# Performance work log

Measured on AMD Instinct MI355X. Metric: run time of the kernel, lower is better.

The kernel has to match this reference:

```python
import jax, jax.numpy as jnp
import numpy as np

D_EMB = 1024
D_HEAD = 64
B = 4
T = 4096


def setup_inputs() -> dict:
    key = jax.random.key(0)
    kx, kk, kq, kv = jax.random.split(key, 4)
    s = 1.0 / np.sqrt(D_EMB)  # torch Linear default init scale (uniform bound)
    x = jax.random.normal(kx, (B, T, D_EMB), dtype=jnp.float32)
    Wk = jax.random.uniform(kk, (D_HEAD, D_EMB), jnp.float32, -s, s)
    Wq = jax.random.uniform(kq, (D_HEAD, D_EMB), jnp.float32, -s, s)
    Wv = jax.random.uniform(kv, (D_HEAD, D_EMB), jnp.float32, -s, s)
    return {"x": x, "Wk": Wk, "Wq": Wq, "Wv": Wv}


def reference(x, Wk, Wq, Wv):
    # x: (B, T, d_emb); W*: (d_head, d_emb) -- torch Linear stores (out, in)
    k = jnp.einsum('bte,he->bth', x, Wk)
    q = jnp.einsum('bte,he->bth', x, Wq)
    v = jnp.einsum('bte,he->bth', x, Wv)
    scale = D_HEAD ** (-0.5)
    a = jnp.einsum('bth,bsh->bts', q, k) * scale  # (B, T, T)
    Tlen = x.shape[-2]
    causal = jnp.tril(jnp.ones((Tlen, Tlen), dtype=bool))
    a = jnp.where(causal, a, -jnp.inf)
    a = jax.nn.softmax(a, axis=-1)
    return jnp.einsum('bts,bsh->bth', a, v)  # (B, T, d_head)
```

## Files before the change

### kernel.cpp

```cpp
#include <hip/hip_runtime.h>
#include <hip/hip_bf16.h>

#define D_EMB 1024
#define T_LEN 4096
#define NTASK 1088

typedef short short8 __attribute__((ext_vector_type(8)));
typedef float f32x4 __attribute__((ext_vector_type(4)));
typedef float f32x16 __attribute__((ext_vector_type(16)));
typedef float float4v __attribute__((ext_vector_type(4)));

__device__ __forceinline__ unsigned short f32_to_bf16(float f) {
    union { float f; unsigned int u; } c; c.f = f;
    unsigned int u = c.u;
    return (unsigned short)((u + 0x7FFFu + ((u >> 16) & 1u)) >> 16);
}
__device__ __forceinline__ float bf16_to_f32(unsigned short v) {
    union { unsigned int u; float f; } c; c.u = ((unsigned int)v) << 16;
    return c.f;
}
__device__ __forceinline__ unsigned cvtpk_bf16(float a, float b) {
    unsigned r;
    asm("v_cvt_pk_bf16_f32 %0, %1, %2" : "=v"(r) : "v"(a), "v"(b));
    return r;
}
__device__ __forceinline__ void gl_lds16(const void* g, void* l) {
    __builtin_amdgcn_global_load_lds(
        (const __attribute__((address_space(1))) unsigned int*)(g),
        (__attribute__((address_space(3))) unsigned int*)(l), 16, 0, 0);
}

#define QSCALE (0.125f * 1.44269504f)

__global__ __launch_bounds__(256) void convert_w(const float* __restrict__ Wk,
                                                 const float* __restrict__ Wq,
                                                 const float* __restrict__ Wv,
                                                 unsigned short* __restrict__ Wb) {
    int e = (blockIdx.x * 256 + threadIdx.x) * 8;
    const float* src;
    if (e < 65536) src = Wk + e;
    else if (e < 131072) src = Wq + (e - 65536);
    else src = Wv + (e - 131072);
    float4v a0 = *(const float4v*)src;
    float4v a1 = *(const float4v*)(src + 4);
    short8 r;
    r[0] = (short)f32_to_bf16(a0[0]); r[1] = (short)f32_to_bf16(a0[1]);
    r[2] = (short)f32_to_bf16(a0[2]); r[3] = (short)f32_to_bf16(a0[3]);
    r[4] = (short)f32_to_bf16(a1[0]); r[5] = (short)f32_to_bf16(a1[1]);
    r[6] = (short)f32_to_bf16(a1[2]); r[7] = (short)f32_to_bf16(a1[3]);
    int row = e >> 10;
    int dst = e ^ ((row & 7) << 3);
    *(short8*)(Wb + dst) = r;
}

__global__ __launch_bounds__(256, 2) void qkv_proj(const float* __restrict__ x,
                                                   const unsigned short* __restrict__ Wb,
                                                   unsigned short* __restrict__ Kb,
                                                   unsigned short* __restrict__ Qb,
                                                   unsigned short* __restrict__ Vt) {
    __shared__ __attribute__((aligned(16))) unsigned short Wsl[2][12288];

    int tid = threadIdx.x;
    int lane = tid & 63, wave = tid >> 6;
    int lo = lane & 15, hi = lane >> 4;
    int rg = wave >> 1, nh = wave & 1;
    int row0 = blockIdx.x * 32;

    const float* xp = x + (size_t)(row0 + rg * 16 + lo) * D_EMB + hi * 8;

    f32x4 acc[6];
#pragma unroll
    for (int i = 0; i < 6; i++) acc[i] = (f32x4){0.f, 0.f, 0.f, 0.f};

    float4v xa0 = *(const float4v*)(xp);
    float4v xa1 = *(const float4v*)(xp + 4);
    float4v xa2 = *(const float4v*)(xp + 32);
    float4v xa3 = *(const float4v*)(xp + 36);
    float4v xb0 = *(const float4v*)(xp + 64);
    float4v xb1 = *(const float4v*)(xp + 68);
    float4v xb2 = *(const float4v*)(xp + 96);
    float4v xb3 = *(const float4v*)(xp + 100);

#pragma unroll
    for (int j = 0; j < 6; j++) {
        int unit = j * 4 + wave;
        int u = unit * 64 + lane;
        gl_lds16(Wb + (size_t)(u >> 3) * D_EMB + (u & 7) * 8, &Wsl[0][unit * 512]);
    }
    __syncthreads();

    int buf = 0;
    int xorm = (lo & 7) << 4;
    int rowbase = nh * 96 + lo;

    for (int kt = 0; kt < 16; kt++) {
        int ktn = (kt < 14) ? kt + 2 : 15;
        const float* pn = xp + ktn * 64;
        float4v xc0 = *(const float4v*)(pn);
        float4v xc1 = *(const float4v*)(pn + 4);
        float4v xc2 = *(const float4v*)(pn + 32);
        float4v xc3 = *(const float4v*)(pn + 36);

        if (kt < 15) {
            int k0n = (kt + 1) * 64;
#pragma unroll
            for (int j = 0; j < 6; j++) {
                int unit = j * 4 + wave;
                int u = unit * 64 + lane;
                gl_lds16(Wb + (size_t)(u >> 3) * D_EMB + k0n + (u & 7) * 8,
                         &Wsl[buf ^ 1][unit * 512]);
            }
        }

        short8 af[2];
        {
            union { unsigned u[4]; short8 s; } c;
            c.u[0] = cvtpk_bf16(xa0[0], xa0[1]);
            c.u[1] = cvtpk_bf16(xa0[2], xa0[3]);
            c.u[2] = cvtpk_bf16(xa1[0], xa1[1]);
            c.u[3] = cvtpk_bf16(xa1[2], xa1[3]);
            af[0] = c.s;
            c.u[0] = cvtpk_bf16(xa2[0], xa2[1]);
            c.u[1] = cvtpk_bf16(xa2[2], xa2[3]);
            c.u[2] = cvtpk_bf16(xa3[0], xa3[1]);
            c.u[3] = cvtpk_bf16(xa3[2], xa3[3]);
            af[1] = c.s;
        }

        const char* sb = (const char*)&Wsl[buf][0];
#pragma unroll
        for (int i = 0; i < 6; i++) {
            int row = rowbase + i * 16;
#pragma unroll
            for (int ks = 0; ks < 2; ks++) {
                short8 bfrag = *(const short8*)(sb + row * 128 + ((ks * 64 + hi * 16) ^ xorm));
                acc[i] = __builtin_amdgcn_mfma_f32_16x16x32_bf16(af[ks], bfrag, acc[i], 0, 0, 0);
            }
        }
        __syncthreads();
        buf ^= 1;
        xa0 = xb0; xa1 = xb1; xa2 = xb2; xa3 = xb3;
        xb0 = xc0; xb1 = xc1; xb2 = xc2; xb3 = xc3;
    }

#pragma unroll
    for (int i = 0; i < 6; i++) {
        int n = nh * 6 + i;
#pragma unroll
        for (int r = 0; r < 4; r++) {
            int grow = row0 + rg * 16 + hi * 4 + r;
            float val = acc[i][r];
            if (n < 4) {
                Kb[(size_t)grow * 64 + n * 16 + lo] = f32_to_bf16(val);
            } else if (n < 8) {
                Qb[(size_t)grow * 64 + (n - 4) * 16 + lo] = f32_to_bf16(val * QSCALE);
            } else {
                int bb = grow >> 12;
                Vt[((size_t)bb * 64 + (n - 8) * 16 + lo) * T_LEN + (grow & 4095)] = f32_to_bf16(val);
            }
        }
    }
}

__global__ __launch_bounds__(64, 4) void attn(const unsigned short* __restrict__ Qb,
                                              const unsigned short* __restrict__ Kb,
                                              const unsigned short* __restrict__ Vt,
                                              unsigned short* __restrict__ Opart,
                                              float* __restrict__ Mpart,
                                              float* __restrict__ Lpart) {
    int lane = threadIdx.x;
    int q32 = lane & 31;
    int hi = lane >> 5;
    unsigned lin = blockIdx.x;
    int b = lin & 3;
    int s = (int)(((lin >> 3) << 1) | ((lin >> 2) & 1));

    int k = 15, rem = s;
    while (rem >= 8 * (k + 1)) { rem -= 8 * (k + 1); k--; }
    int cpt = k + 1;
    int ti = rem / cpt;
    int t = (k << 3) + 7 - ti;
    int c = rem - ti * cpt;

    int u0 = c * 8;
    int u1 = min(u0 + 8, t + 1);

    size_t base = (size_t)b * T_LEN;
    int qg = t * 32 + q32;

    short8 qf[4];
    const unsigned short* qp = Qb + (base + qg) * 64 + hi * 8;
#pragma unroll
    for (int d = 0; d < 4; d++) qf[d] = *(const short8*)(qp + d * 16);

    size_t vbase = ((size_t)b * 64 + q32) * T_LEN;
    f32x16 o0 = {0.f}, o1 = {0.f};
    float m = -3e38f, l = 0.f;

    for (int u = u0; u < u1; ++u) {
        const unsigned short* kp = Kb + (base + u * 32 + q32) * 64 + hi * 8;
        short8 kc0 = *(const short8*)kp;
        short8 kc1 = *(const short8*)(kp + 16);
        short8 kc2 = *(const short8*)(kp + 32);
        short8 kc3 = *(const short8*)(kp + 48);
        const unsigned short* vp = Vt + vbase + u * 32 + hi * 8;
        short8 vc0 = *(const short8*)vp;
        short8 vc1 = *(const short8*)(vp + 16);
        short8 vc2 = *(const short8*)(vp + 32 * T_LEN);
        short8 vc3 = *(const short8*)(vp + 32 * T_LEN + 16);

        f32x16 sc = {0.f};
        sc = __builtin_amdgcn_mfma_f32_32x32x16_bf16(kc0, qf[0], sc, 0, 0, 0);
        sc = __builtin_amdgcn_mfma_f32_32x32x16_bf16(kc1, qf[1], sc, 0, 0, 0);
        sc = __builtin_amdgcn_mfma_f32_32x32x16_bf16(kc2, qf[2], sc, 0, 0, 0);
        sc = __builtin_amdgcn_mfma_f32_32x32x16_bf16(kc3, qf[3], sc, 0, 0, 0);

        if (u == t) {
#pragma unroll
            for (int r = 0; r < 16; ++r) {
                int ko = (r & 3) + 8 * (r >> 2) + 4 * hi;
                sc[r] = (ko <= q32) ? sc[r] : -3e38f;
            }
        }

        float t0 = fmaxf(fmaxf(sc[0], sc[1]), sc[2]);
        float t1 = fmaxf(fmaxf(sc[3], sc[4]), sc[5]);
        float t2 = fmaxf(fmaxf(sc[6], sc[7]), sc[8]);
        float t3 = fmaxf(fmaxf(sc[9], sc[10]), sc[11]);
        float t4 = fmaxf(fmaxf(sc[12], sc[13]), sc[14]);
        float t5 = fmaxf(fmaxf(t0, t1), sc[15]);
        float t6 = fmaxf(fmaxf(t2, t3), t4);
        float mx = fmaxf(t5, t6);
        mx = fmaxf(mx, __shfl_xor(mx, 32));

        if (__any(mx > m + 8.0f)) {
            float mn = fmaxf(m, mx);
            float al = exp2f(m - mn);
            m = mn; l *= al;
#pragma unroll
            for (int r = 0; r < 16; ++r) { o0[r] *= al; o1[r] *= al; }
        }

#pragma unroll
        for (int r = 0; r < 16; ++r) sc[r] = exp2f(sc[r] - m);
        float y0 = (sc[0] + sc[8]) + (sc[4] + sc[12]);
        float y1 = (sc[1] + sc[9]) + (sc[5] + sc[13]);
        float y2 = (sc[2] + sc[10]) + (sc[6] + sc[14]);
        float y3 = (sc[3] + sc[11]) + (sc[7] + sc[15]);
        float sum = (y0 + y1) + (y2 + y3);
        sum += __shfl_xor(sum, 32);
        l += sum;

        unsigned bb0, bb1, bb2, bb3, bb4, bb5, bb6, bb7;
        bb0 = cvtpk_bf16(sc[0],  sc[1]);
        bb1 = cvtpk_bf16(sc[2],  sc[3]);
        bb2 = cvtpk_bf16(sc[4],  sc[5]);
        bb3 = cvtpk_bf16(sc[6],  sc[7]);
        bb4 = cvtpk_bf16(sc[8],  sc[9]);
        bb5 = cvtpk_bf16(sc[10], sc[11]);
        bb6 = cvtpk_bf16(sc[12], sc[13]);
        bb7 = cvtpk_bf16(sc[14], sc[15]);
        asm("v_permlane32_swap_b32 %0, %1" : "+v"(bb0), "+v"(bb2));
        asm("v_permlane32_swap_b32 %0, %1" : "+v"(bb1), "+v"(bb3));
        asm("v_permlane32_swap_b32 %0, %1" : "+v"(bb4), "+v"(bb6));
        asm("v_permlane32_swap_b32 %0, %1" : "+v"(bb5), "+v"(bb7));
        union U8 { unsigned u[4]; short8 s; };
        U8 p0; p0.u[0] = bb0; p0.u[1] = bb1; p0.u[2] = bb2; p0.u[3] = bb3;
        U8 p1; p1.u[0] = bb4; p1.u[1] = bb5; p1.u[2] = bb6; p1.u[3] = bb7;

        o0 = __builtin_amdgcn_mfma_f32_32x32x16_bf16(vc0, p0.s, o0, 0, 0, 0);
        o0 = __builtin_amdgcn_mfma_f32_32x32x16_bf16(vc1, p1.s, o0, 0, 0, 0);
        o1 = __builtin_amdgcn_mfma_f32_32x32x16_bf16(vc2, p0.s, o1, 0, 0, 0);
        o1 = __builtin_amdgcn_mfma_f32_32x32x16_bf16(vc3, p1.s, o1, 0, 0, 0);
    }

    size_t tbase = ((size_t)(b * NTASK + s) * 32 + q32) * 64;
#pragma unroll
    for (int hb = 0; hb < 2; hb++) {
#pragma unroll
        for (int g = 0; g < 4; g++) {
            float e0 = hb ? o1[4 * g] : o0[4 * g];
            float e1 = hb ? o1[4 * g + 1] : o0[4 * g + 1];
            float e2 = hb ? o1[4 * g + 2] : o0[4 * g + 2];
            float e3 = hb ? o1[4 * g + 3] : o0[4 * g + 3];
            unsigned w0 = cvtpk_bf16(e0, e1);
            unsigned w1 = cvtpk_bf16(e2, e3);
            int h0 = hb * 32 + g * 8 + hi * 4;
            *reinterpret_cast<uint2*>(Opart + tbase + h0) = make_uint2(w0, w1);
        }
    }
    if (lane < 32) {
        Mpart[(b * NTASK + s) * 32 + q32] = m;
        Lpart[(b * NTASK + s) * 32 + q32] = l;
    }
}

__global__ __launch_bounds__(256) void attn_merge(const unsigned short* __restrict__ Opart,
                                                  const float* __restrict__ Mpart,
                                                  const float* __restrict__ Lpart,
                                                  float* __restrict__ out) {
    int tid = threadIdx.x;
    int g = blockIdx.x * 64 + (tid >> 2);
    int h0 = (tid & 3) * 16;
    int b = g >> 12, t = g & 4095;
    int tile = t >> 5, r32 = t & 31;
    int k = tile >> 3;
    int nch = k + 1;
    int s0 = 8 * (136 - (((k + 1) * (k + 2)) >> 1)) + (7 - (tile & 7)) * nch;
    int tb = b * NTASK + s0;

    float mm = -3e38f;
    for (int i = 0; i < nch; i++) mm = fmaxf(mm, Mpart[(tb + i) * 32 + r32]);
    float ll = 0.f;
    float acc[16];
#pragma unroll
    for (int e = 0; e < 16; e++) acc[e] = 0.f;
    for (int i = 0; i < nch; i++) {
        float a = exp2f(Mpart[(tb + i) * 32 + r32] - mm);
        ll += a * Lpart[(tb + i) * 32 + r32];
        const unsigned short* op = Opart + ((size_t)(tb + i) * 32 + r32) * 64 + h0;
        short8 v0 = *(const short8*)op;
        short8 v1 = *(const short8*)(op + 8);
#pragma unroll
        for (int e = 0; e < 8; e++) {
            acc[e]     += a * bf16_to_f32((unsigned short)v0[e]);
            acc[8 + e] += a * bf16_to_f32((unsigned short)v1[e]);
        }
    }
    float inv = 1.f / ll;
    float* dst = out + (size_t)g * 64 + h0;
#pragma unroll
    for (int e = 0; e < 16; e++) dst[e] = acc[e] * inv;
}

extern "C" void kernel_launch(void* const* d_in, const int* in_sizes, int n_in,
                              void* d_out, int out_size, void* d_ws, size_t ws_size,
                              hipStream_t stream) {
    (void)in_sizes; (void)n_in; (void)out_size; (void)ws_size;
    const float* x  = (const float*)d_in[0];
    const float* Wk = (const float*)d_in[1];
    const float* Wq = (const float*)d_in[2];
    const float* Wv = (const float*)d_in[3];
    float* out = (float*)d_out;

    unsigned short* Wb = (unsigned short*)d_ws;
    unsigned short* Kb = Wb + 196608;
    unsigned short* Qb = Kb + 1048576;
    unsigned short* Vt = Qb + 1048576;
    unsigned short* Opart = Vt + 1048576;
    float* Mpart = (float*)(Opart + (size_t)4 * NTASK * 32 * 64);
    float* Lpart = Mpart + 4 * NTASK * 32;

    hipLaunchKernelGGL(convert_w, dim3(96), dim3(256), 0, stream, Wk, Wq, Wv, Wb);
    hipLaunchKernelGGL(qkv_proj, dim3(512), dim3(256), 0, stream, x, Wb, Kb, Qb, Vt);
    hipLaunchKernelGGL(attn, dim3(4 * NTASK), dim3(64), 0, stream, Qb, Kb, Vt, Opart, Mpart, Lpart);
    hipLaunchKernelGGL(attn_merge, dim3(256), dim3(256), 0, stream, Opart, Mpart, Lpart, out);
}
```

Baseline: 93.14 us.

## Process two 32-row query tiles per attention wave to reuse K/V loads

Each attention wave now handles a 64-row query supertile, two 32-row tiles, instead of one. Every K and V chunk loaded from global memory feeds MFMAs for both tiles, halving K/V traffic per query and giving the scheduler independent MFMA chains to interleave. The task decomposition, causal masking, partial-result slot layout and merge indexing are rewritten to match. The cost is roughly double the register pressure, reflected in launch bounds dropping from 4 to 2 waves. Half as many blocks are launched, each doing some wasted masked work on the diagonal chunk for tile A.

```diff
diff --git a/kernel.cpp b/kernel.cpp
--- a/kernel.cpp
+++ b/kernel.cpp
@@ -3,7 +3,7 @@
 
 #define D_EMB 1024
 #define T_LEN 4096
-#define NTASK 1088
+#define NTASK2 544
 
 typedef short short8 __attribute__((ext_vector_type(8)));
 typedef float f32x4 __attribute__((ext_vector_type(4)));
@@ -23,6 +23,12 @@
     unsigned r;
     asm("v_cvt_pk_bf16_f32 %0, %1, %2" : "=v"(r) : "v"(a), "v"(b));
     return r;
+}
+__device__ __forceinline__ float xhalf_max(float x) {
+    return fmaxf(x, __shfl_xor(x, 32));
+}
+__device__ __forceinline__ float xhalf_add(float x) {
+    return x + __shfl_xor(x, 32);
 }
 __device__ __forceinline__ void gl_lds16(const void* g, void* l) {
     __builtin_amdgcn_global_load_lds(
@@ -162,7 +168,7 @@
     }
 }
 
-__global__ __launch_bounds__(64, 4) void attn(const unsigned short* __restrict__ Qb,
+__global__ __launch_bounds__(64, 2) void attn(const unsigned short* __restrict__ Qb,
                                               const unsigned short* __restrict__ Kb,
                                               const unsigned short* __restrict__ Vt,
                                               unsigned short* __restrict__ Opart,
@@ -175,27 +181,32 @@
     int b = lin & 3;
     int s = (int)(((lin >> 3) << 1) | ((lin >> 2) & 1));
 
-    int k = 15, rem = s;
-    while (rem >= 8 * (k + 1)) { rem -= 8 * (k + 1); k--; }
-    int cpt = k + 1;
-    int ti = rem / cpt;
-    int t = (k << 3) + 7 - ti;
-    int c = rem - ti * cpt;
+    int k = 16, rem = s;
+    while (rem >= 4 * k) { rem -= 4 * k; k--; }
+    int ti = rem / k;
+    int st = 4 * k - 1 - ti;
+    int c = rem - ti * k;
 
     int u0 = c * 8;
-    int u1 = min(u0 + 8, t + 1);
+    int u1 = min(u0 + 8, 2 * st + 2);
+    int ta = 2 * st, tb = ta + 1;
+    int qrowA = 64 * st + q32;
+    int qrowB = qrowA + 32;
 
     size_t base = (size_t)b * T_LEN;
-    int qg = t * 32 + q32;
-
-    short8 qf[4];
-    const unsigned short* qp = Qb + (base + qg) * 64 + hi * 8;
-#pragma unroll
-    for (int d = 0; d < 4; d++) qf[d] = *(const short8*)(qp + d * 16);
+
+    short8 qfa[4], qfb[4];
+    const unsigned short* qpa = Qb + (base + qrowA) * 64 + hi * 8;
+    const unsigned short* qpb = Qb + (base + qrowB) * 64 + hi * 8;
+#pragma unroll
+    for (int d = 0; d < 4; d++) {
+        qfa[d] = *(const short8*)(qpa + d * 16);
+        qfb[d] = *(const short8*)(qpb + d * 16);
+    }
 
     size_t vbase = ((size_t)b * 64 + q32) * T_LEN;
-    f32x16 o0 = {0.f}, o1 = {0.f};
-    float m = -3e38f, l = 0.f;
+    f32x16 oA0 = {0.f}, oA1 = {0.f}, oB0 = {0.f}, oB1 = {0.f};
+    float mA = -3e38f, lA = 0.f, mB = -3e38f, lB = 0.f;
 
     for (int u = u0; u < u1; ++u) {
         const unsigned short* kp = Kb + (base + u * 32 + q32) * 64 + hi * 8;
@@ -209,89 +220,134 @@
         short8 vc2 = *(const short8*)(vp + 32 * T_LEN);
         short8 vc3 = *(const short8*)(vp + 32 * T_LEN + 16);
 
-        f32x16 sc = {0.f};
-        sc = __builtin_amdgcn_mfma_f32_32x32x16_bf16(kc0, qf[0], sc, 0, 0, 0);
-        sc = __builtin_amdgcn_mfma_f32_32x32x16_bf16(kc1, qf[1], sc, 0, 0, 0);
-        sc = __builtin_amdgcn_mfma_f32_32x32x16_bf16(kc2, qf[2], sc, 0, 0, 0);
-        sc = __builtin_amdgcn_mfma_f32_32x32x16_bf16(kc3, qf[3], sc, 0, 0, 0);
-
-        if (u == t) {
+        f32x16 sa = {0.f}, sb = {0.f};
+        sa = __builtin_amdgcn_mfma_f32_32x32x16_bf16(kc0, qfa[0], sa, 0, 0, 0);
+        sb = __builtin_amdgcn_mfma_f32_32x32x16_bf16(kc0, qfb[0], sb, 0, 0, 0);
+        sa = __builtin_amdgcn_mfma_f32_32x32x16_bf16(kc1, qfa[1], sa, 0, 0, 0);
+        sb = __builtin_amdgcn_mfma_f32_32x32x16_bf16(kc1, qfb[1], sb, 0, 0, 0);
+        sa = __builtin_amdgcn_mfma_f32_32x32x16_bf16(kc2, qfa[2], sa, 0, 0, 0);
+        sb = __builtin_amdgcn_mfma_f32_32x32x16_bf16(kc2, qfb[2], sb, 0, 0, 0);
+        sa = __builtin_amdgcn_mfma_f32_32x32x16_bf16(kc3, qfa[3], sa, 0, 0, 0);
+        sb = __builtin_amdgcn_mfma_f32_32x32x16_bf16(kc3, qfb[3], sb, 0, 0, 0);
+
+        if (u >= ta) {
 #pragma unroll
             for (int r = 0; r < 16; ++r) {
-                int ko = (r & 3) + 8 * (r >> 2) + 4 * hi;
-                sc[r] = (ko <= q32) ? sc[r] : -3e38f;
+                int key = 32 * u + (r & 3) + 8 * (r >> 2) + 4 * hi;
+                sa[r] = (key <= qrowA) ? sa[r] : -3e38f;
+                if (u == tb) sb[r] = (key <= qrowB) ? sb[r] : -3e38f;
             }
         }
 
-        float t0 = fmaxf(fmaxf(sc[0], sc[1]), sc[2]);
-        float t1 = fmaxf(fmaxf(sc[3], sc[4]), sc[5]);
-        float t2 = fmaxf(fmaxf(sc[6], sc[7]), sc[8]);
-        float t3 = fmaxf(fmaxf(sc[9], sc[10]), sc[11]);
-        float t4 = fmaxf(fmaxf(sc[12], sc[13]), sc[14]);
-        float t5 = fmaxf(fmaxf(t0, t1), sc[15]);
-        float t6 = fmaxf(fmaxf(t2, t3), t4);
-        float mx = fmaxf(t5, t6);
-        mx = fmaxf(mx, __shfl_xor(mx, 32));
-
-        if (__any(mx > m + 8.0f)) {
-            float mn = fmaxf(m, mx);
-            float al = exp2f(m - mn);
-            m = mn; l *= al;
-#pragma unroll
-            for (int r = 0; r < 16; ++r) { o0[r] *= al; o1[r] *= al; }
-        }
-
-#pragma unroll
-        for (int r = 0; r < 16; ++r) sc[r] = exp2f(sc[r] - m);
-        float y0 = (sc[0] + sc[8]) + (sc[4] + sc[12]);
-        float y1 = (sc[1] + sc[9]) + (sc[5] + sc[13]);
-        float y2 = (sc[2] + sc[10]) + (sc[6] + sc[14]);
-        float y3 = (sc[3] + sc[11]) + (sc[7] + sc[15]);
-        float sum = (y0 + y1) + (y2 + y3);
-        sum += __shfl_xor(sum, 32);
-        l += sum;
-
-        unsigned bb0, bb1, bb2, bb3, bb4, bb5, bb6, bb7;
-        bb0 = cvtpk_bf16(sc[0],  sc[1]);
-        bb1 = cvtpk_bf16(sc[2],  sc[3]);
-        bb2 = cvtpk_bf16(sc[4],  sc[5]);
-        bb3 = cvtpk_bf16(sc[6],  sc[7]);
-        bb4 = cvtpk_bf16(sc[8],  sc[9]);
-        bb5 = cvtpk_bf16(sc[10], sc[11]);
-        bb6 = cvtpk_bf16(sc[12], sc[13]);
-        bb7 = cvtpk_bf16(sc[14], sc[15]);
-        asm("v_permlane32_swap_b32 %0, %1" : "+v"(bb0), "+v"(bb2));
-        asm("v_permlane32_swap_b32 %0, %1" : "+v"(bb1), "+v"(bb3));
-        asm("v_permlane32_swap_b32 %0, %1" : "+v"(bb4), "+v"(bb6));
-        asm("v_permlane32_swap_b32 %0, %1" : "+v"(bb5), "+v"(bb7));
+        float a0 = fmaxf(fmaxf(sa[0], sa[1]), sa[2]);
+        float a1 = fmaxf(fmaxf(sa[3], sa[4]), sa[5]);
+        float a2 = fmaxf(fmaxf(sa[6], sa[7]), sa[8]);
+        float a3 = fmaxf(fmaxf(sa[9], sa[10]), sa[11]);
+        float a4 = fmaxf(fmaxf(sa[12], sa[13]), sa[14]);
+        float mxA = fmaxf(fmaxf(fmaxf(a0, a1), fmaxf(a2, a3)), fmaxf(a4, sa[15]));
+        float b0 = fmaxf(fmaxf(sb[0], sb[1]), sb[2]);
+        float b1 = fmaxf(fmaxf(sb[3], sb[4]), sb[5]);
+        float b2 = fmaxf(fmaxf(sb[6], sb[7]), sb[8]);
+        float b3 = fmaxf(fmaxf(sb[9], sb[10]), sb[11]);
+        float b4 = fmaxf(fmaxf(sb[12], sb[13]), sb[14]);
+        float mxB = fmaxf(fmaxf(fmaxf(b0, b1), fmaxf(b2, b3)), fmaxf(b4, sb[15]));
+        mxA = xhalf_max(mxA);
+        mxB = xhalf_max(mxB);
+
+        float grow = fmaxf(mxA - mA, mxB - mB);
+        if (__any(grow > 8.0f)) {
+            float mnA = fmaxf(mA, mxA);
+            float alA = exp2f(mA - mnA);
+            mA = mnA; lA *= alA;
+            float mnB = fmaxf(mB, mxB);
+            float alB = exp2f(mB - mnB);
+            mB = mnB; lB *= alB;
+#pragma unroll
+            for (int r = 0; r < 16; ++r) {
+                oA0[r] *= alA; oA1[r] *= alA;
+                oB0[r] *= alB; oB1[r] *= alB;
+            }
+        }
+
+#pragma unroll
+        for (int r = 0; r < 16; ++r) {
+            sa[r] = exp2f(sa[r] - mA);
+            sb[r] = exp2f(sb[r] - mB);
+        }
+        float yA = ((sa[0] + sa[8]) + (sa[4] + sa[12])) + ((sa[1] + sa[9]) + (sa[5] + sa[13]))
+                 + ((sa[2] + sa[10]) + (sa[6] + sa[14])) + ((sa[3] + sa[11]) + (sa[7] + sa[15]));
+        float yB = ((sb[0] + sb[8]) + (sb[4] + sb[12])) + ((sb[1] + sb[9]) + (sb[5] + sb[13]))
+                 + ((sb[2] + sb[10]) + (sb[6] + sb[14])) + ((sb[3] + sb[11]) + (sb[7] + sb[15]));
+        lA += xhalf_add(yA);
+        lB += xhalf_add(yB);
+
+        unsigned pa0 = cvtpk_bf16(sa[0],  sa[1]);
+        unsigned pa1 = cvtpk_bf16(sa[2],  sa[3]);
+        unsigned pa2 = cvtpk_bf16(sa[4],  sa[5]);
+        unsigned pa3 = cvtpk_bf16(sa[6],  sa[7]);
+        unsigned pa4 = cvtpk_bf16(sa[8],  sa[9]);
+        unsigned pa5 = cvtpk_bf16(sa[10], sa[11]);
+        unsigned pa6 = cvtpk_bf16(sa[12], sa[13]);
+        unsigned pa7 = cvtpk_bf16(sa[14], sa[15]);
+        unsigned pb0 = cvtpk_bf16(sb[0],  sb[1]);
+        unsigned pb1 = cvtpk_bf16(sb[2],  sb[3]);
+        unsigned pb2 = cvtpk_bf16(sb[4],  sb[5]);
+        unsigned pb3 = cvtpk_bf16(sb[6],  sb[7]);
+        unsigned pb4 = cvtpk_bf16(sb[8],  sb[9]);
+        unsigned pb5 = cvtpk_bf16(sb[10], sb[11]);
+        unsigned pb6 = cvtpk_bf16(sb[12], sb[13]);
+        unsigned pb7 = cvtpk_bf16(sb[14], sb[15]);
+        asm("v_permlane32_swap_b32 %0, %1" : "+v"(pa0), "+v"(pa2));
+        asm("v_permlane32_swap_b32 %0, %1" : "+v"(pa1), "+v"(pa3));
+        asm("v_permlane32_swap_b32 %0, %1" : "+v"(pa4), "+v"(pa6));
+        asm("v_permlane32_swap_b32 %0, %1" : "+v"(pa5), "+v"(pa7));
+        asm("v_permlane32_swap_b32 %0, %1" : "+v"(pb0), "+v"(pb2));
+        asm("v_permlane32_swap_b32 %0, %1" : "+v"(pb1), "+v"(pb3));
+        asm("v_permlane32_swap_b32 %0, %1" : "+v"(pb4), "+v"(pb6));
+        asm("v_permlane32_swap_b32 %0, %1" : "+v"(pb5), "+v"(pb7));
         union U8 { unsigned u[4]; short8 s; };
-        U8 p0; p0.u[0] = bb0; p0.u[1] = bb1; p0.u[2] = bb2; p0.u[3] = bb3;
-        U8 p1; p1.u[0] = bb4; p1.u[1] = bb5; p1.u[2] = bb6; p1.u[3] = bb7;
-
-        o0 = __builtin_amdgcn_mfma_f32_32x32x16_bf16(vc0, p0.s, o0, 0, 0, 0);
-        o0 = __builtin_amdgcn_mfma_f32_32x32x16_bf16(vc1, p1.s, o0, 0, 0, 0);
-        o1 = __builtin_amdgcn_mfma_f32_32x32x16_bf16(vc2, p0.s, o1, 0, 0, 0);
-        o1 = __builtin_amdgcn_mfma_f32_32x32x16_bf16(vc3, p1.s, o1, 0, 0, 0);
-    }
-
-    size_t tbase = ((size_t)(b * NTASK + s) * 32 + q32) * 64;
+        U8 fA0; fA0.u[0] = pa0; fA0.u[1] = pa1; fA0.u[2] = pa2; fA0.u[3] = pa3;
+        U8 fA1; fA1.u[0] = pa4; fA1.u[1] = pa5; fA1.u[2] = pa6; fA1.u[3] = pa7;
+        U8 fB0; fB0.u[0] = pb0; fB0.u[1] = pb1; fB0.u[2] = pb2; fB0.u[3] = pb3;
+        U8 fB1; fB1.u[0] = pb4; fB1.u[1] = pb5; fB1.u[2] = pb6; fB1.u[3] = pb7;
+
+        oA0 = __builtin_amdgcn_mfma_f32_32x32x16_bf16(vc0, fA0.s, oA0, 0, 0, 0);
+        oB0 = __builtin_amdgcn_mfma_f32_32x32x16_bf16(vc0, fB0.s, oB0, 0, 0, 0);
+        oA0 = __builtin_amdgcn_mfma_f32_32x32x16_bf16(vc1, fA1.s, oA0, 0, 0, 0);
+        oB0 = __builtin_amdgcn_mfma_f32_32x32x16_bf16(vc1, fB1.s, oB0, 0, 0, 0);
+        oA1 = __builtin_amdgcn_mfma_f32_32x32x16_bf16(vc2, fA0.s, oA1, 0, 0, 0);
+        oB1 = __builtin_amdgcn_mfma_f32_32x32x16_bf16(vc2, fB0.s, oB1, 0, 0, 0);
+        oA1 = __builtin_amdgcn_mfma_f32_32x32x16_bf16(vc3, fA1.s, oA1, 0, 0, 0);
+        oB1 = __builtin_amdgcn_mfma_f32_32x32x16_bf16(vc3, fB1.s, oB1, 0, 0, 0);
+    }
+
+    int slotA = (b * NTASK2 + s) * 2;
+    size_t tbA = ((size_t)slotA * 32 + q32) * 64;
+    size_t tbB = ((size_t)(slotA + 1) * 32 + q32) * 64;
 #pragma unroll
     for (int hb = 0; hb < 2; hb++) {
 #pragma unroll
         for (int g = 0; g < 4; g++) {
-            float e0 = hb ? o1[4 * g] : o0[4 * g];
-            float e1 = hb ? o1[4 * g + 1] : o0[4 * g + 1];
-            float e2 = hb ? o1[4 * g + 2] : o0[4 * g + 2];
-            float e3 = hb ? o1[4 * g + 3] : o0[4 * g + 3];
-            unsigned w0 = cvtpk_bf16(e0, e1);
-            unsigned w1 = cvtpk_bf16(e2, e3);
+            float eA0 = hb ? oA1[4 * g] : oA0[4 * g];
+            float eA1 = hb ? oA1[4 * g + 1] : oA0[4 * g + 1];
+            float eA2 = hb ? oA1[4 * g + 2] : oA0[4 * g + 2];
+            float eA3 = hb ? oA1[4 * g + 3] : oA0[4 * g + 3];
+            float eB0 = hb ? oB1[4 * g] : oB0[4 * g];
+            float eB1 = hb ? oB1[4 * g + 1] : oB0[4 * g + 1];
+            float eB2 = hb ? oB1[4 * g + 2] : oB0[4 * g + 2];
+            float eB3 = hb ? oB1[4 * g + 3] : oB0[4 * g + 3];
             int h0 = hb * 32 + g * 8 + hi * 4;
-            *reinterpret_cast<uint2*>(Opart + tbase + h0) = make_uint2(w0, w1);
+            *reinterpret_cast<uint2*>(Opart + tbA + h0) =
+                make_uint2(cvtpk_bf16(eA0, eA1), cvtpk_bf16(eA2, eA3));
+            *reinterpret_cast<uint2*>(Opart + tbB + h0) =
+                make_uint2(cvtpk_bf16(eB0, eB1), cvtpk_bf16(eB2, eB3));
         }
     }
     if (lane < 32) {
-        Mpart[(b * NTASK + s) * 32 + q32] = m;
-        Lpart[(b * NTASK + s) * 32 + q32] = l;
+        Mpart[slotA * 32 + q32] = mA;
+        Lpart[slotA * 32 + q32] = lA;
+        Mpart[(slotA + 1) * 32 + q32] = mB;
+        Lpart[(slotA + 1) * 32 + q32] = lB;
     }
 }
 
@@ -303,22 +359,25 @@
     int g = blockIdx.x * 64 + (tid >> 2);
     int h0 = (tid & 3) * 16;
     int b = g >> 12, t = g & 4095;
-    int tile = t >> 5, r32 = t & 31;
-    int k = tile >> 3;
-    int nch = k + 1;
-    int s0 = 8 * (136 - (((k + 1) * (k + 2)) >> 1)) + (7 - (tile & 7)) * nch;
-    int tb = b * NTASK + s0;
+    int tile32 = t >> 5, r32 = t & 31;
+    int st = tile32 >> 1, member = tile32 & 1;
+    int k = (st >> 2) + 1;
+    int sbase = 4 * (136 - ((k * (k + 1)) >> 1));
+    int ti = 4 * k - 1 - st;
+    int s0 = sbase + ti * k;
+    int slot0 = (b * NTASK2 + s0) * 2 + member;
 
     float mm = -3e38f;
-    for (int i = 0; i < nch; i++) mm = fmaxf(mm, Mpart[(tb + i) * 32 + r32]);
+    for (int i = 0; i < k; i++) mm = fmaxf(mm, Mpart[(slot0 + 2 * i) * 32 + r32]);
     float ll = 0.f;
     float acc[16];
 #pragma unroll
     for (int e = 0; e < 16; e++) acc[e] = 0.f;
-    for (int i = 0; i < nch; i++) {
-        float a = exp2f(Mpart[(tb + i) * 32 + r32] - mm);
-        ll += a * Lpart[(tb + i) * 32 + r32];
-        const unsigned short* op = Opart + ((size_t)(tb + i) * 32 + r32) * 64 + h0;
+    for (int i = 0; i < k; i++) {
+        int slot = slot0 + 2 * i;
+        float a = exp2f(Mpart[slot * 32 + r32] - mm);
+        ll += a * Lpart[slot * 32 + r32];
+        const unsigned short* op = Opart + ((size_t)slot * 32 + r32) * 64 + h0;
         short8 v0 = *(const short8*)op;
         short8 v1 = *(const short8*)(op + 8);
 #pragma unroll
@@ -348,11 +407,11 @@
     unsigned short* Qb = Kb + 1048576;
     unsigned short* Vt = Qb + 1048576;
     unsigned short* Opart = Vt + 1048576;
-    float* Mpart = (float*)(Opart + (size_t)4 * NTASK * 32 * 64);
-    float* Lpart = Mpart + 4 * NTASK * 32;
+    float* Mpart = (float*)(Opart + (size_t)4 * NTASK2 * 2 * 32 * 64);
+    float* Lpart = Mpart + 4 * NTASK2 * 2 * 32;
 
     hipLaunchKernelGGL(convert_w, dim3(96), dim3(256), 0, stream, Wk, Wq, Wv, Wb);
     hipLaunchKernelGGL(qkv_proj, dim3(512), dim3(256), 0, stream, x, Wb, Kb, Qb, Vt);
-    hipLaunchKernelGGL(attn, dim3(4 * NTASK), dim3(64), 0, stream, Qb, Kb, Vt, Opart, Mpart, Lpart);
+    hipLaunchKernelGGL(attn, dim3(4 * NTASK2), dim3(64), 0, stream, Qb, Kb, Vt, Opart, Mpart, Lpart);
     hipLaunchKernelGGL(attn_merge, dim3(256), dim3(256), 0, stream, Opart, Mpart, Lpart, out);
 }
```

Measured after the change: 81.81 us. -12.2%, faster.
